# Kernel optimization log

Measured on AMD Instinct MI355X. Metric: run time of the kernel, lower is better.

Reference implementation:

```python
import jax, jax.numpy as jnp
import numpy as np

N_HEADS = 16
D_EMBED = 1024
D_HEAD = D_EMBED // N_HEADS  # 64
B, S = 2, 2048


def setup_inputs() -> dict:
    key = jax.random.key(0)
    ks = jax.random.split(key, 6)
    k = jax.random.normal(ks[0], (B, S, D_EMBED), dtype=jnp.float32)
    q = jax.random.normal(ks[1], (B, S, D_EMBED), dtype=jnp.float32)
    v = jax.random.normal(ks[2], (B, S, D_EMBED), dtype=jnp.float32)
    # per-head projections, shared across heads (nn.Linear(d_head, d_head, bias=False))
    scale = 1.0 / np.sqrt(D_HEAD)
    Wk = jax.random.normal(ks[3], (D_HEAD, D_HEAD), dtype=jnp.float32) * scale
    Wq = jax.random.normal(ks[4], (D_HEAD, D_HEAD), dtype=jnp.float32) * scale
    Wv = jax.random.normal(ks[5], (D_HEAD, D_HEAD), dtype=jnp.float32) * scale
    return {"k": k, "q": q, "v": v, "Wk": Wk, "Wq": Wq, "Wv": Wv}


def reference(k, q, v, Wk, Wq, Wv):
    b, s, _ = k.shape
    # split heads: [b, s, h, dh]
    kh = k.reshape(b, s, N_HEADS, D_HEAD)
    qh = q.reshape(b, s, N_HEADS, D_HEAD)
    vh = v.reshape(b, s, N_HEADS, D_HEAD)
    # shared per-head linear projection (y = x @ W^T, torch Linear convention)
    kh = jnp.einsum('bshd,ed->bshe', kh, Wk)
    qh = jnp.einsum('bshd,ed->bshe', qh, Wq)
    vh = jnp.einsum('bshd,ed->bshe', vh, Wv)
    # attention scores [b, h, q, k]
    scores = jnp.einsum('bqhd,bkhd->bhqk', qh, kh) / np.sqrt(D_HEAD).astype(np.float32)
    attn = jax.nn.softmax(scores, axis=-1)
    out = jnp.einsum('bhqk,bkhd->bqhd', attn, vh)
    return out.reshape(b, s, D_EMBED)
```

## Files before the change

kernel.cpp:

```cpp
#include <hip/hip_runtime.h>
#include <hip/hip_bf16.h>

typedef unsigned short u16;
typedef __bf16 bf16x8 __attribute__((ext_vector_type(8)));
typedef float f32x4 __attribute__((ext_vector_type(4)));

#define S_LEN 2048
#define NH 16
#define NB 2
#define HEAD_ELEMS (NB * NH * S_LEN * 64)
#define BH_ELEMS (S_LEN * 64)

#if __has_builtin(__builtin_amdgcn_exp2f)
#define EXP2(x) __builtin_amdgcn_exp2f(x)
#else
#define EXP2(x) exp2f(x)
#endif

#define QSCALE 0.180336880f
#define SHIFT2 30.0f

__device__ __forceinline__ bf16x8 pack8(float4 a, float4 b, float sc) {
    union { bf16x8 v; __hip_bfloat162 h[4]; } r;
    r.h[0] = __float22bfloat162_rn(make_float2(a.x * sc, a.y * sc));
    r.h[1] = __float22bfloat162_rn(make_float2(a.z * sc, a.w * sc));
    r.h[2] = __float22bfloat162_rn(make_float2(b.x * sc, b.y * sc));
    r.h[3] = __float22bfloat162_rn(make_float2(b.z * sc, b.w * sc));
    return r.v;
}

__global__ __launch_bounds__(256) void proj_fused(
    const float* __restrict__ kin, const float* __restrict__ qin,
    const float* __restrict__ vin,
    const float* __restrict__ Wk, const float* __restrict__ Wq,
    const float* __restrict__ Wv,
    u16* __restrict__ Kh, u16* __restrict__ Qh, u16* __restrict__ Vt)
{
    __shared__ __align__(16) u16 Yld[8 * 16 * 72];
    __shared__ __align__(16) u16 Stage[16 * 512];

    const int tid = threadIdx.x;
    const int wave = tid >> 6;
    const int lane = tid & 63;
    const int quad = lane >> 4;
    const int l15 = lane & 15;
    const int bid = blockIdx.x;

    if (bid < 1024) {
        const int stile = bid & 255;
        const int p = (bid >> 8) & 1;
        const int hh = bid >> 9;
        const long row0 = (long)stile * 16;
        const int b = (int)(row0 >> 11);
        const int s0 = (int)(row0 & 2047);

        const float* X = p ? qin : kin;
        const float* W = p ? Wq : Wk;
        const float sc = p ? QSCALE : 1.0f;

        #pragma unroll
        for (int it = 0; it < 4; ++it) {
            int chunk = tid + it * 256;
            int row = chunk >> 6, col8 = chunk & 63;
            const float* gp = X + (row0 + row) * 1024 + hh * 512 + col8 * 8;
            bf16x8 v = pack8(*(const float4*)gp, *(const float4*)(gp + 4), 1.0f);
            int byteoff = (row * 1024 + col8 * 16) ^ ((row & 7) << 4);
            *(bf16x8*)((char*)Stage + byteoff) = v;
        }

        bf16x8 wf[4][2];
        #pragma unroll
        for (int nt = 0; nt < 4; ++nt) {
            const float* wr = W + (nt * 16 + l15) * 64 + quad * 8;
            wf[nt][0] = pack8(*(const float4*)(wr),      *(const float4*)(wr + 4),  sc);
            wf[nt][1] = pack8(*(const float4*)(wr + 32), *(const float4*)(wr + 36), sc);
        }
        __syncthreads();

        #pragma unroll
        for (int hp = 0; hp < 2; ++hp) {
            const int hl = wave * 2 + hp;
            int acol = l15 * 1024 + hl * 128 + quad * 16;
            int swz = (l15 & 7) << 4;
            bf16x8 a0 = *(const bf16x8*)((const char*)Stage + (acol ^ swz));
            bf16x8 a1 = *(const bf16x8*)((const char*)Stage + ((acol + 64) ^ swz));
            #pragma unroll
            for (int nt = 0; nt < 4; ++nt) {
                f32x4 c = (f32x4){0.f, 0.f, 0.f, 0.f};
                c = __builtin_amdgcn_mfma_f32_16x16x32_bf16(a0, wf[nt][0], c, 0, 0, 0);
                c = __builtin_amdgcn_mfma_f32_16x16x32_bf16(a1, wf[nt][1], c, 0, 0, 0);
                union { __hip_bfloat162 h2; u16 u[2]; } x01, x23;
                x01.h2 = __float22bfloat162_rn(make_float2(c[0], c[1]));
                x23.h2 = __float22bfloat162_rn(make_float2(c[2], c[3]));
                int base = (hl * 16 + quad * 4) * 72 + nt * 16 + l15;
                Yld[base]       = x01.u[0];
                Yld[base + 72]  = x01.u[1];
                Yld[base + 144] = x23.u[0];
                Yld[base + 216] = x23.u[1];
            }
        }
        __syncthreads();

        if (p) {
            #pragma unroll
            for (int it = 0; it < 4; ++it) {
                int idx = tid + it * 256;
                int eg = idx & 7, s = (idx >> 3) & 15, hl = idx >> 7;
                int bh = b * NH + hh * 8 + hl;
                *(float4*)(Qh + ((long)bh * S_LEN + s0 + s) * 64 + eg * 8) =
                    *(const float4*)&Yld[(hl * 16 + s) * 72 + eg * 8];
            }
        } else {
            #pragma unroll
            for (int it = 0; it < 4; ++it) {
                int idx = tid + it * 256;
                int eg = idx & 7, s = (idx >> 3) & 15, hl = idx >> 7;
                int bh = b * NH + hh * 8 + hl;
                int sg = s0 + s;
                int kt = sg >> 6, c = (sg >> 5) & 1, rp = sg & 31;
                int nn = (rp >> 2) & 1;
                int l15p = ((rp >> 3) << 2) | (rp & 3);
                int j = eg >> 2, qd = eg & 3;
                long off = (long)bh * BH_ELEMS
                         + (long)((((kt * 2 + c) * 2 + nn) * 2 + j) * 512 + (qd * 16 + l15p) * 8);
                *(float4*)(Kh + off) = *(const float4*)&Yld[(hl * 16 + s) * 72 + eg * 8];
            }
        }
    } else {
        const int vid = bid - 1024;
        const long row0 = (long)(vid & 63) * 64;
        const int b = (int)(row0 >> 11);
        const int s0 = (int)(row0 & 2047);
        const int h = vid >> 6;
        const int bh = b * NH + h;
        const int kt = s0 >> 6;

        #pragma unroll
        for (int it = 0; it < 4; ++it) {
            int chunk = tid + it * 256;
            int row = chunk >> 4, c16 = chunk & 15;
            const float* gp = vin + (row0 + row) * 1024 + h * 64 + c16 * 4;
            float4 f = *(const float4*)gp;
            union { __hip_bfloat162 h2[2]; unsigned long long u; } pk;
            pk.h2[0] = __float22bfloat162_rn(make_float2(f.x, f.y));
            pk.h2[1] = __float22bfloat162_rn(make_float2(f.z, f.w));
            int byteoff = (row * 128 + c16 * 8) ^ ((row & 7) << 4);
            *(unsigned long long*)((char*)Stage + byteoff) = pk.u;
        }

        bf16x8 wf[4][2];
        #pragma unroll
        for (int dt = 0; dt < 4; ++dt) {
            const float* wr = Wv + (dt * 16 + l15) * 64 + quad * 8;
            wf[dt][0] = pack8(*(const float4*)(wr),      *(const float4*)(wr + 4),  1.0f);
            wf[dt][1] = pack8(*(const float4*)(wr + 32), *(const float4*)(wr + 36), 1.0f);
        }
        __syncthreads();

        int vcol = (wave * 16 + l15) * 128 + quad * 16;
        int vswz = (l15 & 7) << 4;
        bf16x8 x0 = *(const bf16x8*)((const char*)Stage + (vcol ^ vswz));
        bf16x8 x1 = *(const bf16x8*)((const char*)Stage + ((vcol + 64) ^ vswz));

        #pragma unroll
        for (int dt = 0; dt < 4; ++dt) {
            f32x4 c = (f32x4){0.f, 0.f, 0.f, 0.f};
            c = __builtin_amdgcn_mfma_f32_16x16x32_bf16(wf[dt][0], x0, c, 0, 0, 0);
            c = __builtin_amdgcn_mfma_f32_16x16x32_bf16(wf[dt][1], x1, c, 0, 0, 0);
            int base = (dt * 16 + quad * 4) * 72 + wave * 16 + l15;
            union { __hip_bfloat162 h2; u16 u[2]; } x01, x23;
            x01.h2 = __float22bfloat162_rn(make_float2(c[0], c[1]));
            x23.h2 = __float22bfloat162_rn(make_float2(c[2], c[3]));
            Yld[base]       = x01.u[0];
            Yld[base + 72]  = x01.u[1];
            Yld[base + 144] = x23.u[0];
            Yld[base + 216] = x23.u[1];
        }
        __syncthreads();

        u16* dstb = Vt + (long)bh * BH_ELEMS;
        #pragma unroll
        for (int it = 0; it < 2; ++it) {
            int idx = tid + it * 256;
            int sg = idx & 7, e_row = idx >> 3;
            int c = sg >> 2, lhi = sg & 3;
            int dt = e_row >> 4, l15p = e_row & 15;
            long off = (long)(((kt * 2 + c) * 4 + dt) * 512 + (lhi * 16 + l15p) * 8);
            *(float4*)(dstb + off) = *(const float4*)&Yld[e_row * 72 + sg * 8];
        }
    }
}

__global__ __launch_bounds__(256, 2) void attn_kernel(
    const u16* __restrict__ Qh, const u16* __restrict__ Kh,
    const u16* __restrict__ Vt, float* __restrict__ out)
{
    __shared__ __align__(16) u16 Qld[64 * 72];
    __shared__ __align__(16) float Old[4][64 * 20];
    __shared__ float lbc[4][64];

    const int tid = threadIdx.x;
    const int wave = tid >> 6;
    const int lane = tid & 63;
    const int quad = lane >> 4;
    const int l15 = lane & 15;
    const int bid = blockIdx.x;
    const int xcd = bid & 7;
    const int i = bid >> 3;
    const int bh = xcd * 4 + (i >> 5);
    const int qb = i & 31;
    const int b = bh >> 4, h = bh & 15;
    const int q0 = qb * 64;
    const u16* kb = Kh + (long)bh * BH_ELEMS + lane * 8;
    const u16* vb = Vt + (long)bh * BH_ELEMS + lane * 8;

    {
        const u16* qp = Qh + ((long)bh * S_LEN + q0) * 64;
        #pragma unroll
        for (int i2 = 0; i2 < 2; ++i2) {
            int idx = tid + i2 * 256;
            int row = idx >> 3, gg = idx & 7;
            *(float4*)&Qld[row * 72 + gg * 8] = *(const float4*)(qp + row * 64 + gg * 8);
        }
    }
    __syncthreads();

    f32x4 oacc[4][4];
    #pragma unroll
    for (int g = 0; g < 4; ++g)
        #pragma unroll
        for (int dt = 0; dt < 4; ++dt) oacc[g][dt] = (f32x4){0.f, 0.f, 0.f, 0.f};
    float rs[4] = {0.f, 0.f, 0.f, 0.f};

    for (int kt = wave; kt < S_LEN / 64; kt += 4) {
        const u16* kt_k = kb + kt * 4096;
        const u16* kt_v = vb + kt * 4096;
        #pragma unroll
        for (int c = 0; c < 2; ++c) {
            bf16x8 kf[2][2], vf[4];
            kf[0][0] = *(const bf16x8*)(kt_k + c * 2048);
            kf[0][1] = *(const bf16x8*)(kt_k + c * 2048 + 512);
            kf[1][0] = *(const bf16x8*)(kt_k + c * 2048 + 1024);
            kf[1][1] = *(const bf16x8*)(kt_k + c * 2048 + 1536);
            #pragma unroll
            for (int dt = 0; dt < 4; ++dt)
                vf[dt] = *(const bf16x8*)(kt_v + c * 2048 + dt * 512);

            #pragma unroll
            for (int g = 0; g < 4; ++g) {
                const u16* qrow = &Qld[(g * 16 + l15) * 72 + quad * 8];
                bf16x8 qb0 = *(const bf16x8*)(qrow);
                bf16x8 qb1 = *(const bf16x8*)(qrow + 32);
                f32x4 s0 = (f32x4){-SHIFT2, -SHIFT2, -SHIFT2, -SHIFT2};
                f32x4 s1 = (f32x4){-SHIFT2, -SHIFT2, -SHIFT2, -SHIFT2};
                s0 = __builtin_amdgcn_mfma_f32_16x16x32_bf16(kf[0][0], qb0, s0, 0, 0, 0);
                s0 = __builtin_amdgcn_mfma_f32_16x16x32_bf16(kf[0][1], qb1, s0, 0, 0, 0);
                s1 = __builtin_amdgcn_mfma_f32_16x16x32_bf16(kf[1][0], qb0, s1, 0, 0, 0);
                s1 = __builtin_amdgcn_mfma_f32_16x16x32_bf16(kf[1][1], qb1, s1, 0, 0, 0);

                float p00 = EXP2(s0[0]), p01 = EXP2(s0[1]);
                float p02 = EXP2(s0[2]), p03 = EXP2(s0[3]);
                float p10 = EXP2(s1[0]), p11 = EXP2(s1[1]);
                float p12 = EXP2(s1[2]), p13 = EXP2(s1[3]);
                rs[g] += ((p00 + p01) + (p02 + p03)) + ((p10 + p11) + (p12 + p13));

                union { bf16x8 v; __hip_bfloat162 h2[4]; } pf;
                pf.h2[0] = __float22bfloat162_rn(make_float2(p00, p01));
                pf.h2[1] = __float22bfloat162_rn(make_float2(p02, p03));
                pf.h2[2] = __float22bfloat162_rn(make_float2(p10, p11));
                pf.h2[3] = __float22bfloat162_rn(make_float2(p12, p13));

                #pragma unroll
                for (int dt = 0; dt < 4; ++dt)
                    oacc[g][dt] = __builtin_amdgcn_mfma_f32_16x16x32_bf16(vf[dt], pf.v, oacc[g][dt], 0, 0, 0);
            }
        }
    }

    #pragma unroll
    for (int g = 0; g < 4; ++g) {
        rs[g] += __shfl_xor(rs[g], 16);
        rs[g] += __shfl_xor(rs[g], 32);
    }
    if (lane < 16) {
        #pragma unroll
        for (int g = 0; g < 4; ++g) lbc[wave][g * 16 + lane] = rs[g];
    }
    __syncthreads();

    const int rq = tid >> 2, seg = tid & 3;
    const float linv = 1.0f / (lbc[0][rq] + lbc[1][rq] + lbc[2][rq] + lbc[3][rq]);
    float* op = out + ((long)(b * S_LEN + q0 + rq)) * 1024 + h * 64;

    #pragma unroll
    for (int ph = 0; ph < 4; ++ph) {
        #pragma unroll
        for (int g = 0; g < 4; ++g)
            *(f32x4*)&Old[wave][(g * 16 + l15) * 20 + quad * 4] = oacc[g][ph];
        __syncthreads();
        f32x4 a = (f32x4){0.f, 0.f, 0.f, 0.f};
        #pragma unroll
        for (int w = 0; w < 4; ++w) a += *(const f32x4*)&Old[w][rq * 20 + seg * 4];
        *(float4*)(op + ph * 16 + seg * 4) =
            make_float4(a[0] * linv, a[1] * linv, a[2] * linv, a[3] * linv);
        __syncthreads();
    }
}

extern "C" void kernel_launch(void* const* d_in, const int* in_sizes, int n_in,
                              void* d_out, int out_size, void* d_ws, size_t ws_size,
                              hipStream_t stream) {
    const float* kin = (const float*)d_in[0];
    const float* qin = (const float*)d_in[1];
    const float* vin = (const float*)d_in[2];
    const float* Wk  = (const float*)d_in[3];
    const float* Wq  = (const float*)d_in[4];
    const float* Wv  = (const float*)d_in[5];
    float* out = (float*)d_out;

    u16* wsp = (u16*)d_ws;
    u16* Kh = wsp;
    u16* Qh = wsp + (long)HEAD_ELEMS;
    u16* Vt = wsp + 2 * (long)HEAD_ELEMS;

    proj_fused<<<dim3(2048), 256, 0, stream>>>(kin, qin, vin, Wk, Wq, Wv, Kh, Qh, Vt);
    attn_kernel<<<dim3(1024), 256, 0, stream>>>(Qh, Kh, Vt, out);
}
```

Baseline: 146.8 us.

## Split attention across query rows per wave with double-buffered LDS K/V tiles

Each wave now owns 16 query rows and walks all key tiles, instead of each wave owning a quarter of the key tiles for all 64 queries. K/V tiles are staged cooperatively into a double-buffered LDS array with direct global-to-LDS loads, prefetching the next tile while the current one is computed. This removes the cross-wave output reduction through shared memory and its barriers, and cuts per-wave register use so occupancy can go to 4 blocks per SM. The cost is a block-wide barrier on every key tile and LDS read traffic for K/V.

```diff
diff --git a/kernel.cpp b/kernel.cpp
--- a/kernel.cpp
+++ b/kernel.cpp
@@ -19,6 +19,10 @@
 
 #define QSCALE 0.180336880f
 #define SHIFT2 30.0f
+
+#define GLDS16(g, l) __builtin_amdgcn_global_load_lds( \
+    (const __attribute__((address_space(1))) void*)(g), \
+    (__attribute__((address_space(3))) void*)(l), 16, 0, 0)
 
 __device__ __forceinline__ bf16x8 pack8(float4 a, float4 b, float sc) {
     union { bf16x8 v; __hip_bfloat162 h[4]; } r;
@@ -191,13 +195,11 @@
     }
 }
 
-__global__ __launch_bounds__(256, 2) void attn_kernel(
+__global__ __launch_bounds__(256, 4) void attn_kernel(
     const u16* __restrict__ Qh, const u16* __restrict__ Kh,
     const u16* __restrict__ Vt, float* __restrict__ out)
 {
-    __shared__ __align__(16) u16 Qld[64 * 72];
-    __shared__ __align__(16) float Old[4][64 * 20];
-    __shared__ float lbc[4][64];
+    __shared__ __align__(16) u16 KV[2][8192];
 
     const int tid = threadIdx.x;
     const int wave = tid >> 6;
@@ -211,99 +213,95 @@
     const int qb = i & 31;
     const int b = bh >> 4, h = bh & 15;
     const int q0 = qb * 64;
-    const u16* kb = Kh + (long)bh * BH_ELEMS + lane * 8;
-    const u16* vb = Vt + (long)bh * BH_ELEMS + lane * 8;
-
+    const u16* kb = Kh + (long)bh * BH_ELEMS;
+    const u16* vb = Vt + (long)bh * BH_ELEMS;
+
+    bf16x8 qf0, qf1;
     {
-        const u16* qp = Qh + ((long)bh * S_LEN + q0) * 64;
-        #pragma unroll
-        for (int i2 = 0; i2 < 2; ++i2) {
-            int idx = tid + i2 * 256;
-            int row = idx >> 3, gg = idx & 7;
-            *(float4*)&Qld[row * 72 + gg * 8] = *(const float4*)(qp + row * 64 + gg * 8);
-        }
+        const u16* qp = Qh + ((long)bh * S_LEN + q0 + wave * 16 + l15) * 64 + quad * 8;
+        qf0 = *(const bf16x8*)(qp);
+        qf1 = *(const bf16x8*)(qp + 32);
+    }
+
+    const u16* gsk = ((wave & 2) ? vb : kb) + ((wave & 1) << 11) + lane * 8;
+    const int ldsoff = ((wave & 2) ? 4096 : 0) + ((wave & 1) << 11);
+
+    f32x4 oacc[4];
+    #pragma unroll
+    for (int dt = 0; dt < 4; ++dt) oacc[dt] = (f32x4){0.f, 0.f, 0.f, 0.f};
+    float rs = 0.f;
+
+    {
+        const u16* g = gsk;
+        u16* l = &KV[0][ldsoff];
+        #pragma unroll
+        for (int ii = 0; ii < 4; ++ii)
+            GLDS16(g + ii * 512, l + ii * 512);
     }
     __syncthreads();
 
-    f32x4 oacc[4][4];
-    #pragma unroll
-    for (int g = 0; g < 4; ++g)
-        #pragma unroll
-        for (int dt = 0; dt < 4; ++dt) oacc[g][dt] = (f32x4){0.f, 0.f, 0.f, 0.f};
-    float rs[4] = {0.f, 0.f, 0.f, 0.f};
-
-    for (int kt = wave; kt < S_LEN / 64; kt += 4) {
-        const u16* kt_k = kb + kt * 4096;
-        const u16* kt_v = vb + kt * 4096;
+    int buf = 0;
+    #pragma unroll 1
+    for (int t = 0; t < S_LEN / 64; ++t) {
+        if (t < S_LEN / 64 - 1) {
+            const u16* g = gsk + (t + 1) * 4096;
+            u16* l = &KV[buf ^ 1][ldsoff];
+            #pragma unroll
+            for (int ii = 0; ii < 4; ++ii)
+                GLDS16(g + ii * 512, l + ii * 512);
+        }
+
+        const u16* Kl = &KV[buf][0];
+        const u16* Vl = &KV[buf][4096];
         #pragma unroll
         for (int c = 0; c < 2; ++c) {
             bf16x8 kf[2][2], vf[4];
-            kf[0][0] = *(const bf16x8*)(kt_k + c * 2048);
-            kf[0][1] = *(const bf16x8*)(kt_k + c * 2048 + 512);
-            kf[1][0] = *(const bf16x8*)(kt_k + c * 2048 + 1024);
-            kf[1][1] = *(const bf16x8*)(kt_k + c * 2048 + 1536);
+            #pragma unroll
+            for (int nn = 0; nn < 2; ++nn) {
+                kf[nn][0] = *(const bf16x8*)(Kl + ((c * 2 + nn) * 2 + 0) * 512 + lane * 8);
+                kf[nn][1] = *(const bf16x8*)(Kl + ((c * 2 + nn) * 2 + 1) * 512 + lane * 8);
+            }
             #pragma unroll
             for (int dt = 0; dt < 4; ++dt)
-                vf[dt] = *(const bf16x8*)(kt_v + c * 2048 + dt * 512);
-
-            #pragma unroll
-            for (int g = 0; g < 4; ++g) {
-                const u16* qrow = &Qld[(g * 16 + l15) * 72 + quad * 8];
-                bf16x8 qb0 = *(const bf16x8*)(qrow);
-                bf16x8 qb1 = *(const bf16x8*)(qrow + 32);
-                f32x4 s0 = (f32x4){-SHIFT2, -SHIFT2, -SHIFT2, -SHIFT2};
-                f32x4 s1 = (f32x4){-SHIFT2, -SHIFT2, -SHIFT2, -SHIFT2};
-                s0 = __builtin_amdgcn_mfma_f32_16x16x32_bf16(kf[0][0], qb0, s0, 0, 0, 0);
-                s0 = __builtin_amdgcn_mfma_f32_16x16x32_bf16(kf[0][1], qb1, s0, 0, 0, 0);
-                s1 = __builtin_amdgcn_mfma_f32_16x16x32_bf16(kf[1][0], qb0, s1, 0, 0, 0);
-                s1 = __builtin_amdgcn_mfma_f32_16x16x32_bf16(kf[1][1], qb1, s1, 0, 0, 0);
-
-                float p00 = EXP2(s0[0]), p01 = EXP2(s0[1]);
-                float p02 = EXP2(s0[2]), p03 = EXP2(s0[3]);
-                float p10 = EXP2(s1[0]), p11 = EXP2(s1[1]);
-                float p12 = EXP2(s1[2]), p13 = EXP2(s1[3]);
-                rs[g] += ((p00 + p01) + (p02 + p03)) + ((p10 + p11) + (p12 + p13));
-
-                union { bf16x8 v; __hip_bfloat162 h2[4]; } pf;
-                pf.h2[0] = __float22bfloat162_rn(make_float2(p00, p01));
-                pf.h2[1] = __float22bfloat162_rn(make_float2(p02, p03));
-                pf.h2[2] = __float22bfloat162_rn(make_float2(p10, p11));
-                pf.h2[3] = __float22bfloat162_rn(make_float2(p12, p13));
-
-                #pragma unroll
-                for (int dt = 0; dt < 4; ++dt)
-                    oacc[g][dt] = __builtin_amdgcn_mfma_f32_16x16x32_bf16(vf[dt], pf.v, oacc[g][dt], 0, 0, 0);
-            }
-        }
-    }
-
+                vf[dt] = *(const bf16x8*)(Vl + (c * 4 + dt) * 512 + lane * 8);
+
+            f32x4 s0 = (f32x4){-SHIFT2, -SHIFT2, -SHIFT2, -SHIFT2};
+            f32x4 s1 = (f32x4){-SHIFT2, -SHIFT2, -SHIFT2, -SHIFT2};
+            s0 = __builtin_amdgcn_mfma_f32_16x16x32_bf16(kf[0][0], qf0, s0, 0, 0, 0);
+            s0 = __builtin_amdgcn_mfma_f32_16x16x32_bf16(kf[0][1], qf1, s0, 0, 0, 0);
+            s1 = __builtin_amdgcn_mfma_f32_16x16x32_bf16(kf[1][0], qf0, s1, 0, 0, 0);
+            s1 = __builtin_amdgcn_mfma_f32_16x16x32_bf16(kf[1][1], qf1, s1, 0, 0, 0);
+
+            float p00 = EXP2(s0[0]), p01 = EXP2(s0[1]);
+            float p02 = EXP2(s0[2]), p03 = EXP2(s0[3]);
+            float p10 = EXP2(s1[0]), p11 = EXP2(s1[1]);
+            float p12 = EXP2(s1[2]), p13 = EXP2(s1[3]);
+            rs += ((p00 + p01) + (p02 + p03)) + ((p10 + p11) + (p12 + p13));
+
+            union { bf16x8 v; __hip_bfloat162 h2[4]; } pf;
+            pf.h2[0] = __float22bfloat162_rn(make_float2(p00, p01));
+            pf.h2[1] = __float22bfloat162_rn(make_float2(p02, p03));
+            pf.h2[2] = __float22bfloat162_rn(make_float2(p10, p11));
+            pf.h2[3] = __float22bfloat162_rn(make_float2(p12, p13));
+
+            #pragma unroll
+            for (int dt = 0; dt < 4; ++dt)
+                oacc[dt] = __builtin_amdgcn_mfma_f32_16x16x32_bf16(vf[dt], pf.v, oacc[dt], 0, 0, 0);
+        }
+        __syncthreads();
+        buf ^= 1;
+    }
+
+    rs += __shfl_xor(rs, 16);
+    rs += __shfl_xor(rs, 32);
+    const float linv = 1.0f / rs;
+
+    float* op = out + ((long)(b * S_LEN + q0 + wave * 16 + l15)) * 1024 + h * 64;
     #pragma unroll
-    for (int g = 0; g < 4; ++g) {
-        rs[g] += __shfl_xor(rs[g], 16);
-        rs[g] += __shfl_xor(rs[g], 32);
-    }
-    if (lane < 16) {
-        #pragma unroll
-        for (int g = 0; g < 4; ++g) lbc[wave][g * 16 + lane] = rs[g];
-    }
-    __syncthreads();
-
-    const int rq = tid >> 2, seg = tid & 3;
-    const float linv = 1.0f / (lbc[0][rq] + lbc[1][rq] + lbc[2][rq] + lbc[3][rq]);
-    float* op = out + ((long)(b * S_LEN + q0 + rq)) * 1024 + h * 64;
-
-    #pragma unroll
-    for (int ph = 0; ph < 4; ++ph) {
-        #pragma unroll
-        for (int g = 0; g < 4; ++g)
-            *(f32x4*)&Old[wave][(g * 16 + l15) * 20 + quad * 4] = oacc[g][ph];
-        __syncthreads();
-        f32x4 a = (f32x4){0.f, 0.f, 0.f, 0.f};
-        #pragma unroll
-        for (int w = 0; w < 4; ++w) a += *(const f32x4*)&Old[w][rq * 20 + seg * 4];
-        *(float4*)(op + ph * 16 + seg * 4) =
+    for (int dt = 0; dt < 4; ++dt) {
+        f32x4 a = oacc[dt];
+        *(float4*)(op + dt * 16 + quad * 4) =
             make_float4(a[0] * linv, a[1] * linv, a[2] * linv, a[3] * linv);
-        __syncthreads();
     }
 }
 
```

After: 150.7 us. +2.6%, slower.
